# Kernel optimization log

Measured on AMD Instinct MI355X. Metric: run time of the kernel, lower is better.

The kernel has to match this reference:

```python
import jax, jax.numpy as jnp
import numpy as np

V, D, H, L, B, T = 32000, 1024, 16, 4, 2, 2048
DH = D // H
F = 4 * D
EPS = 1e-5


def setup_inputs() -> dict:
    key = jax.random.key(0)
    ks = jax.random.split(key, 16)
    s = 0.02
    n = lambda k, shape: (jax.random.normal(k, shape, jnp.float32) * s)
    inp = {
        "idx": jax.random.randint(ks[0], (B, T), 0, V, dtype=jnp.int64),
        "tok_emb": n(ks[1], (V, D)),
        "pos_emb": n(ks[2], (1, T, D)),
        # per-layer stacked params; Linear weights stored as (in, out)
        "Wq": n(ks[3], (L, D, D)), "bq": jnp.zeros((L, D)),
        "Wk": n(ks[4], (L, D, D)), "bk": jnp.zeros((L, D)),
        "Wv": n(ks[5], (L, D, D)), "bv": jnp.zeros((L, D)),
        "Wo": n(ks[6], (L, D, D)), "bo": jnp.zeros((L, D)),
        "ln1_g": jnp.ones((L, D)), "ln1_b": jnp.zeros((L, D)),
        "W1": n(ks[7], (L, D, F)), "b1": jnp.zeros((L, F)),
        "W2": n(ks[8], (L, F, D)), "b2": jnp.zeros((L, D)),
        "ln2_g": jnp.ones((L, D)), "ln2_b": jnp.zeros((L, D)),
        "lnf_g": jnp.ones((D,)), "lnf_b": jnp.zeros((D,)),
        "lm_W": n(ks[9], (D, V)),
    }
    return inp


def _ln(x, g, b):
    m = jnp.mean(x, axis=-1, keepdims=True)
    v = jnp.mean(jnp.square(x - m), axis=-1, keepdims=True)
    return (x - m) * jax.lax.rsqrt(v + EPS) * g + b


def _band_attn(x, Wq, bq, Wk, bk, Wv, bv, Wo, bo):
    # width-3 causal band: query t attends to keys {t, t-1, t-2}
    b_, t_, _ = x.shape
    q = (x @ Wq + bq).reshape(b_, t_, H, DH)
    k = (x @ Wk + bk).reshape(b_, t_, H, DH)
    v = (x @ Wv + bv).reshape(b_, t_, H, DH)

    def shift(a, o):  # align key at position t-o with query t
        return jnp.pad(a, ((0, 0), (o, 0), (0, 0), (0, 0)))[:, :t_]

    ks_ = jnp.stack([shift(k, o) for o in range(3)], axis=-2)  # (B,T,H,3,DH)
    vs_ = jnp.stack([shift(v, o) for o in range(3)], axis=-2)
    scale = 1.0 / np.sqrt(DH)
    scores = jnp.einsum('bthd,bthod->btho', q, ks_) * scale       # (B,T,H,3)
    pos = jnp.arange(t_)[None, :, None, None]
    off = jnp.arange(3)[None, None, None, :]
    scores = jnp.where(pos >= off, scores, -jnp.inf)
    p = jax.nn.softmax(scores, axis=-1)
    y = jnp.einsum('btho,bthod->bthd', p, vs_).reshape(b_, t_, D)
    return y @ Wo + bo


def reference(idx, tok_emb, pos_emb, Wq, bq, Wk, bk, Wv, bv, Wo, bo,
              ln1_g, ln1_b, W1, b1, W2, b2, ln2_g, ln2_b, lnf_g, lnf_b, lm_W):
    t_ = idx.shape[1]
    x = tok_emb[idx] + pos_emb[:, :t_, :]
    for i in range(L):
        h = _ln(x, ln1_g[i], ln1_b[i])
        x = x + _band_attn(h, Wq[i], bq[i], Wk[i], bk[i], Wv[i], bv[i], Wo[i], bo[i])
        h = _ln(x, ln2_g[i], ln2_b[i])
        h = jax.nn.gelu(h @ W1[i] + b1[i], approximate=False) @ W2[i] + b2[i]
        x = x + h
    x = _ln(x, lnf_g, lnf_b)
    logits = x @ lm_W
    return logits
```

## Files before the change

kernel.cpp:

```cpp
#include <hip/hip_runtime.h>
#include <cstdint>
#include <cstddef>

#define MROWS   4096
#define TSEQ    2048
#define DMODEL  1024
#define NHEAD   16
#define FFN     4096
#define NVOCAB  32000
#define NLAYER  4

typedef float  f32x4  __attribute__((ext_vector_type(4)));
typedef __bf16 bf16x8 __attribute__((ext_vector_type(8)));

__device__ __forceinline__ unsigned short f2bf(float f) {
    unsigned u = __builtin_bit_cast(unsigned, f);
    u += 0x7fffu + ((u >> 16) & 1u);
    return (unsigned short)(u >> 16);
}
__device__ __forceinline__ float bf2f(unsigned short u) {
    return __builtin_bit_cast(float, (unsigned)u << 16);
}

__device__ __forceinline__ float gelu_exact(float v) {
    return 0.5f * v * (1.0f + erff(v * 0.7071067811865476f));
}

__global__ __launch_bounds__(256) void embed_kernel(const int* __restrict__ idx,
                                                    const float* __restrict__ tok,
                                                    const float* __restrict__ pos,
                                                    float* __restrict__ x) {
    int row = blockIdx.x, tid = threadIdx.x;
    int token = idx[row];
    int t = row & (TSEQ - 1);
    float4 a = ((const float4*)(tok + (size_t)token * DMODEL))[tid];
    float4 p = ((const float4*)(pos + (size_t)t * DMODEL))[tid];
    a.x += p.x; a.y += p.y; a.z += p.z; a.w += p.w;
    ((float4*)(x + (size_t)row * DMODEL))[tid] = a;
}

__global__ __launch_bounds__(256) void ln_kernel(const float* __restrict__ x,
                                                 const float* __restrict__ g,
                                                 const float* __restrict__ b,
                                                 unsigned short* __restrict__ out) {
    int row = blockIdx.x, tid = threadIdx.x;
    float4 v = ((const float4*)(x + (size_t)row * DMODEL))[tid];
    float s1 = v.x + v.y + v.z + v.w;
    float s2 = v.x * v.x + v.y * v.y + v.z * v.z + v.w * v.w;
    for (int s = 32; s; s >>= 1) { s1 += __shfl_xor(s1, s); s2 += __shfl_xor(s2, s); }
    __shared__ float red[8];
    int lane = tid & 63, w = tid >> 6;
    if (lane == 0) { red[w] = s1; red[4 + w] = s2; }
    __syncthreads();
    s1 = red[0] + red[1] + red[2] + red[3];
    s2 = red[4] + red[5] + red[6] + red[7];
    float mean = s1 * (1.0f / DMODEL);
    float var  = s2 * (1.0f / DMODEL) - mean * mean;
    float rs   = rsqrtf(var + 1e-5f);
    float4 gv = ((const float4*)g)[tid];
    float4 bv = ((const float4*)b)[tid];
    size_t o = (size_t)row * DMODEL + tid * 4;
    out[o + 0] = f2bf((v.x - mean) * rs * gv.x + bv.x);
    out[o + 1] = f2bf((v.y - mean) * rs * gv.y + bv.y);
    out[o + 2] = f2bf((v.z - mean) * rs * gv.z + bv.z);
    out[o + 3] = f2bf((v.w - mean) * rs * gv.w + bv.w);
}

__global__ __launch_bounds__(256) void transpose_bf16(const float* __restrict__ W,
                                                      unsigned short* __restrict__ WT,
                                                      int K, int ldW) {
    __shared__ float tile[64][65];
    int n0 = blockIdx.x * 64, k0 = blockIdx.y * 64;
    int tid = threadIdx.x;
    int lr4 = tid & 15;
    int rw  = tid >> 4;
#pragma unroll
    for (int p = 0; p < 4; ++p) {
        int k = rw + p * 16;
        float4 v = *(const float4*)(W + (size_t)(k0 + k) * ldW + n0 + lr4 * 4);
        tile[k][lr4 * 4 + 0] = v.x;
        tile[k][lr4 * 4 + 1] = v.y;
        tile[k][lr4 * 4 + 2] = v.z;
        tile[k][lr4 * 4 + 3] = v.w;
    }
    __syncthreads();
    int kc = tid & 15;
    int nr = tid >> 4;
#pragma unroll
    for (int p = 0; p < 4; ++p) {
        int n = nr + p * 16;
        ushort4 o;
        o.x = f2bf(tile[kc * 4 + 0][n]);
        o.y = f2bf(tile[kc * 4 + 1][n]);
        o.z = f2bf(tile[kc * 4 + 2][n]);
        o.w = f2bf(tile[kc * 4 + 3][n]);
        *(ushort4*)(WT + (size_t)(n0 + n) * K + k0 + kc * 4) = o;
    }
}

__global__ __launch_bounds__(256) void pack_qkv_bias(const float* __restrict__ bq,
                                                     const float* __restrict__ bk,
                                                     const float* __restrict__ bv,
                                                     float* __restrict__ dst) {
    int i = blockIdx.x * 256 + threadIdx.x;
    int l = i / 3072, c = i % 3072;
    float v = (c < 1024) ? bq[l * 1024 + c]
            : (c < 2048) ? bk[l * 1024 + c - 1024]
                         : bv[l * 1024 + c - 2048];
    dst[i] = v;
}

__global__ __launch_bounds__(256) void attn_kernel(const unsigned short* __restrict__ qkv,
                                                   unsigned short* __restrict__ y) {
    int wid  = (blockIdx.x * 256 + threadIdx.x) >> 6;
    int lane = threadIdx.x & 63;
    int h = wid & (NHEAD - 1);
    int row = wid >> 4;
    int t = row & (TSEQ - 1);
    const unsigned short* base = qkv + (size_t)row * 3072 + h * 64;
    float qd = bf2f(base[lane]);
    float d0 = qd * bf2f(base[1024 + lane]);
    float d1 = (t >= 1) ? qd * bf2f(base[1024 - 3072 + lane]) : 0.0f;
    float d2 = (t >= 2) ? qd * bf2f(base[1024 - 6144 + lane]) : 0.0f;
    for (int s = 32; s; s >>= 1) {
        d0 += __shfl_xor(d0, s); d1 += __shfl_xor(d1, s); d2 += __shfl_xor(d2, s);
    }
    d0 *= 0.125f; d1 *= 0.125f; d2 *= 0.125f;
    float m = d0;
    if (t >= 1) m = fmaxf(m, d1);
    if (t >= 2) m = fmaxf(m, d2);
    float p0 = expf(d0 - m);
    float p1 = (t >= 1) ? expf(d1 - m) : 0.0f;
    float p2 = (t >= 2) ? expf(d2 - m) : 0.0f;
    float den = p0 + p1 + p2;
    float v0 = bf2f(base[2048 + lane]);
    float v1 = (t >= 1) ? bf2f(base[2048 - 3072 + lane]) : 0.0f;
    float v2 = (t >= 2) ? bf2f(base[2048 - 6144 + lane]) : 0.0f;
    float yv = (p0 * v0 + p1 * v1 + p2 * v2) / den;
    y[(size_t)row * DMODEL + h * 64 + lane] = f2bf(yv);
}

__device__ __forceinline__ void stage_tile(const unsigned short* __restrict__ g,
                                           unsigned short* s, int K, int tid) {
#pragma unroll
    for (int i = 0; i < 4; ++i) {
        int t2 = tid + i * 512;
        int row = t2 >> 3;
        int col = ((t2 & 7) ^ (row & 7)) * 8;
        __builtin_amdgcn_global_load_lds(
            (const __attribute__((address_space(1))) void*)(g + (size_t)row * K + col),
            (__attribute__((address_space(3))) void*)(s + (size_t)t2 * 8), 16, 0, 0);
    }
}

template <int EPI>
__global__ __launch_bounds__(512, 2) void gemm256(const unsigned short* __restrict__ A,
                                                  const unsigned short* __restrict__ BT,
                                                  const float* __restrict__ bias,
                                                  const float* __restrict__ res,
                                                  float* __restrict__ outF,
                                                  unsigned short* __restrict__ outB,
                                                  int M, int N, int K, int ldc) {
    __shared__ unsigned short As[2][256 * 64];
    __shared__ unsigned short Bs[2][256 * 64];
    const int tid = threadIdx.x;
    const int lane = tid & 63, wid = tid >> 6;
    const int wr = wid >> 2, wc = wid & 3;
    const int lr = lane & 15, kq = lane >> 4;

    const int nbn = N >> 8;
    const int nwg = gridDim.x;
    int orig = blockIdx.x;
    int q8 = nwg >> 3, r8 = nwg & 7;
    int xcd = orig & 7, lin = orig >> 3;
    int wg = (xcd < r8 ? xcd * (q8 + 1) : r8 * (q8 + 1) + (xcd - r8) * q8) + lin;
    int bm = wg / nbn, bn = wg % nbn;

    const unsigned short* Ab = A + (size_t)bm * 256 * K;
    const unsigned short* Bb = BT + (size_t)bn * 256 * K;

    const int aBase = (wr * 128 + lr) * 64;
    const int bBase = (wc * 64 + lr) * 64;
    const int c0 = ((0 * 4 + kq) ^ (lr & 7)) * 8;
    const int c1 = ((1 * 4 + kq) ^ (lr & 7)) * 8;

    f32x4 acc[8][4] = {};
    const int nt = K >> 6;

    stage_tile(Ab, &As[0][0], K, tid);
    stage_tile(Bb, &Bs[0][0], K, tid);
    asm volatile("s_waitcnt vmcnt(0)" ::: "memory");
    __syncthreads();

    for (int t = 0; t < nt; ++t) {
        const unsigned short* sA = &As[t & 1][0];
        const unsigned short* sB = &Bs[t & 1][0];
        unsigned short* dA = &As[(t + 1) & 1][0];
        unsigned short* dB = &Bs[(t + 1) & 1][0];
        const bool pf = (t + 1) < nt;
        const unsigned short* gA = Ab + (size_t)(t + 1) * 64;
        const unsigned short* gB = Bb + (size_t)(t + 1) * 64;

        bf16x8 bfr[4][2];
#pragma unroll
        for (int n = 0; n < 4; ++n) {
            bfr[n][0] = *reinterpret_cast<const bf16x8*>(sB + bBase + n * 16 * 64 + c0);
            bfr[n][1] = *reinterpret_cast<const bf16x8*>(sB + bBase + n * 16 * 64 + c1);
        }

#pragma unroll
        for (int q = 0; q < 4; ++q) {
            bf16x8 af[2][2];
#pragma unroll
            for (int jm = 0; jm < 2; ++jm) {
                const int ro = aBase + (q * 32 + jm * 16) * 64;
                af[jm][0] = *reinterpret_cast<const bf16x8*>(sA + ro + c0);
                af[jm][1] = *reinterpret_cast<const bf16x8*>(sA + ro + c1);
            }
            if (q == 0 && pf) stage_tile(gA, dA, K, tid);
            if (q == 1 && pf) stage_tile(gB, dB, K, tid);
            __builtin_amdgcn_s_barrier();
            __builtin_amdgcn_s_setprio(1);
#pragma unroll
            for (int jm = 0; jm < 2; ++jm)
#pragma unroll
                for (int n = 0; n < 4; ++n) {
                    acc[q * 2 + jm][n] = __builtin_amdgcn_mfma_f32_16x16x32_bf16(af[jm][0], bfr[n][0], acc[q * 2 + jm][n], 0, 0, 0);
                    acc[q * 2 + jm][n] = __builtin_amdgcn_mfma_f32_16x16x32_bf16(af[jm][1], bfr[n][1], acc[q * 2 + jm][n], 0, 0, 0);
                }
            __builtin_amdgcn_s_setprio(0);
            if (q < 3) __builtin_amdgcn_s_barrier();
        }
        asm volatile("s_waitcnt vmcnt(0)" ::: "memory");
        __syncthreads();
    }

    const int row0 = bm * 256 + wr * 128;
    const int col0 = bn * 256 + wc * 64;
#pragma unroll
    for (int m = 0; m < 8; ++m) {
#pragma unroll
        for (int n = 0; n < 4; ++n) {
            int col = col0 + n * 16 + lr;
            int rbase = row0 + m * 16 + kq * 4;
            float bb = bias ? bias[col] : 0.0f;
#pragma unroll
            for (int j = 0; j < 4; ++j) {
                size_t off = (size_t)(rbase + j) * ldc + col;
                float v = acc[m][n][j] + bb;
                if (EPI == 1) v += res[off];
                if (EPI == 2)      outB[off] = f2bf(gelu_exact(v));
                else if (EPI == 3) outB[off] = f2bf(v);
                else               outF[off] = v;
            }
        }
    }
}

__device__ __forceinline__ void stage128(const unsigned short* __restrict__ g,
                                         unsigned short* s, int K, int tid) {
#pragma unroll
    for (int i = 0; i < 2; ++i) {
        int t2 = tid + i * 512;
        int row = t2 >> 3;
        int col = ((t2 & 7) ^ (row & 7)) * 8;
        __builtin_amdgcn_global_load_lds(
            (const __attribute__((address_space(1))) void*)(g + (size_t)row * K + col),
            (__attribute__((address_space(3))) void*)(s + (size_t)t2 * 8), 16, 0, 0);
    }
}

template <int EPI>
__global__ __launch_bounds__(512, 2) void gemm128(const unsigned short* __restrict__ A,
                                                  const unsigned short* __restrict__ BT,
                                                  const float* __restrict__ bias,
                                                  const float* __restrict__ res,
                                                  float* __restrict__ outF,
                                                  unsigned short* __restrict__ outB,
                                                  int M, int N, int K, int ldc) {
    __shared__ unsigned short As[3][128 * 64];
    __shared__ unsigned short Bs[3][128 * 64];
    const int tid = threadIdx.x;
    const int lane = tid & 63, wid = tid >> 6;
    const int wr = wid >> 2, wc = wid & 3;
    const int lr = lane & 15, kq = lane >> 4;

    const int nbn = N >> 7;
    const int nwg = gridDim.x;
    int orig = blockIdx.x;
    int q8 = nwg >> 3, r8 = nwg & 7;
    int xcd = orig & 7, lin = orig >> 3;
    int wg = (xcd < r8 ? xcd * (q8 + 1) : r8 * (q8 + 1) + (xcd - r8) * q8) + lin;
    int bm = wg / nbn, bn = wg % nbn;

    const unsigned short* Ab = A + (size_t)bm * 128 * K;
    const unsigned short* Bb = BT + (size_t)bn * 128 * K;

    const int aBase = (wr * 64 + lr) * 64;
    const int bBase = (wc * 32 + lr) * 64;
    const int c0 = (kq ^ (lr & 7)) * 8;
    const int c1 = ((4 + kq) ^ (lr & 7)) * 8;

    f32x4 acc[4][2] = {};
    const int nt = K >> 6;

    stage128(Ab,      &As[0][0], K, tid);
    stage128(Bb,      &Bs[0][0], K, tid);
    stage128(Ab + 64, &As[1][0], K, tid);
    stage128(Bb + 64, &Bs[1][0], K, tid);
    asm volatile("s_waitcnt vmcnt(4)" ::: "memory");
    __builtin_amdgcn_s_barrier();

    for (int t = 0; t < nt; ++t) {
        const unsigned short* sA = &As[t % 3][0];
        const unsigned short* sB = &Bs[t % 3][0];
        const bool pf = (t + 2) < nt;
        unsigned short* dA = &As[(t + 2) % 3][0];
        unsigned short* dB = &Bs[(t + 2) % 3][0];
        const unsigned short* gA = Ab + (size_t)(t + 2) * 64;
        const unsigned short* gB = Bb + (size_t)(t + 2) * 64;

        bf16x8 bfr[2][2];
#pragma unroll
        for (int n = 0; n < 2; ++n) {
            bfr[n][0] = *reinterpret_cast<const bf16x8*>(sB + bBase + n * 16 * 64 + c0);
            bfr[n][1] = *reinterpret_cast<const bf16x8*>(sB + bBase + n * 16 * 64 + c1);
        }
#pragma unroll
        for (int p = 0; p < 2; ++p) {
            bf16x8 af[2][2];
#pragma unroll
            for (int jm = 0; jm < 2; ++jm) {
                const int ro = aBase + ((p * 2 + jm) * 16) * 64;
                af[jm][0] = *reinterpret_cast<const bf16x8*>(sA + ro + c0);
                af[jm][1] = *reinterpret_cast<const bf16x8*>(sA + ro + c1);
            }
            if (pf && p == 0) stage128(gA, dA, K, tid);
            if (pf && p == 1) stage128(gB, dB, K, tid);
            __builtin_amdgcn_s_barrier();
            __builtin_amdgcn_s_setprio(1);
#pragma unroll
            for (int jm = 0; jm < 2; ++jm)
#pragma unroll
                for (int n = 0; n < 2; ++n) {
                    acc[p * 2 + jm][n] = __builtin_amdgcn_mfma_f32_16x16x32_bf16(af[jm][0], bfr[n][0], acc[p * 2 + jm][n], 0, 0, 0);
                    acc[p * 2 + jm][n] = __builtin_amdgcn_mfma_f32_16x16x32_bf16(af[jm][1], bfr[n][1], acc[p * 2 + jm][n], 0, 0, 0);
                }
            __builtin_amdgcn_s_setprio(0);
        }
        if (t + 1 < nt) {
            if (pf) asm volatile("s_waitcnt vmcnt(4)" ::: "memory");
            else    asm volatile("s_waitcnt vmcnt(0)" ::: "memory");
            __builtin_amdgcn_s_barrier();
        }
    }

    const int row0 = bm * 128 + wr * 64;
    const int col0 = bn * 128 + wc * 32;
#pragma unroll
    for (int m = 0; m < 4; ++m) {
#pragma unroll
        for (int n = 0; n < 2; ++n) {
            int col = col0 + n * 16 + lr;
            int rbase = row0 + m * 16 + kq * 4;
            float bb = bias ? bias[col] : 0.0f;
#pragma unroll
            for (int j = 0; j < 4; ++j) {
                size_t off = (size_t)(rbase + j) * ldc + col;
                float v = acc[m][n][j] + bb;
                if (EPI == 1) v += res[off];
                if (EPI == 2)      outB[off] = f2bf(gelu_exact(v));
                else if (EPI == 3) outB[off] = f2bf(v);
                else               outF[off] = v;
            }
        }
    }
}

extern "C" void kernel_launch(void* const* d_in, const int* in_sizes, int n_in,
                              void* d_out, int out_size, void* d_ws, size_t ws_size,
                              hipStream_t stream) {
    const int*   idx  = (const int*)d_in[0];
    const float* tok  = (const float*)d_in[1];
    const float* pos  = (const float*)d_in[2];
    const float* Wq   = (const float*)d_in[3];
    const float* bq   = (const float*)d_in[4];
    const float* Wk   = (const float*)d_in[5];
    const float* bk   = (const float*)d_in[6];
    const float* Wv   = (const float*)d_in[7];
    const float* bv   = (const float*)d_in[8];
    const float* Wo   = (const float*)d_in[9];
    const float* bo   = (const float*)d_in[10];
    const float* ln1g = (const float*)d_in[11];
    const float* ln1b = (const float*)d_in[12];
    const float* W1   = (const float*)d_in[13];
    const float* b1   = (const float*)d_in[14];
    const float* W2   = (const float*)d_in[15];
    const float* b2   = (const float*)d_in[16];
    const float* ln2g = (const float*)d_in[17];
    const float* ln2b = (const float*)d_in[18];
    const float* lnfg = (const float*)d_in[19];
    const float* lnfb = (const float*)d_in[20];
    const float* lmW  = (const float*)d_in[21];

    char* ws = (char*)d_ws;
    unsigned short* wbuf  = (unsigned short*)(ws);
    unsigned short* hbuf  = (unsigned short*)(ws + (16u << 20));
    unsigned short* ybuf  = (unsigned short*)(ws + (24u << 20));
    unsigned short* xfbuf = (unsigned short*)(ws + (32u << 20));
    float*          bqkv  = (float*)(ws + (40u << 20));

    float* outF = (float*)d_out;
    float* xbuf = outF;
    unsigned short* qkv = (unsigned short*)((char*)d_out + (16ull << 20));
    unsigned short* hidden = (unsigned short*)((char*)d_out + (64ull << 20));

    embed_kernel<<<MROWS, 256, 0, stream>>>(idx, tok, pos, xbuf);
    pack_qkv_bias<<<(NLAYER * 3072) / 256, 256, 0, stream>>>(bq, bk, bv, bqkv);

    for (int l = 0; l < NLAYER; l++) {
        const size_t wl = (size_t)l * DMODEL * DMODEL;
        ln_kernel<<<MROWS, 256, 0, stream>>>(xbuf, ln1g + l * DMODEL, ln1b + l * DMODEL, hbuf);

        transpose_bf16<<<dim3(16, 16), 256, 0, stream>>>(Wq + wl, wbuf,                           DMODEL, DMODEL);
        transpose_bf16<<<dim3(16, 16), 256, 0, stream>>>(Wk + wl, wbuf + (size_t)DMODEL * DMODEL, DMODEL, DMODEL);
        transpose_bf16<<<dim3(16, 16), 256, 0, stream>>>(Wv + wl, wbuf + 2ull * DMODEL * DMODEL,  DMODEL, DMODEL);
        gemm256<3><<<dim3((3072 / 256) * (MROWS / 256)), 512, 0, stream>>>(
            hbuf, wbuf, bqkv + l * 3072, nullptr, nullptr, qkv, MROWS, 3072, DMODEL, 3072);

        attn_kernel<<<MROWS * NHEAD / 4, 256, 0, stream>>>(qkv, ybuf);

        transpose_bf16<<<dim3(16, 16), 256, 0, stream>>>(Wo + wl, wbuf, DMODEL, DMODEL);
        gemm128<1><<<dim3((DMODEL / 128) * (MROWS / 128)), 512, 0, stream>>>(
            ybuf, wbuf, bo + l * DMODEL, xbuf, xbuf, nullptr, MROWS, DMODEL, DMODEL, DMODEL);

        ln_kernel<<<MROWS, 256, 0, stream>>>(xbuf, ln2g + l * DMODEL, ln2b + l * DMODEL, hbuf);

        transpose_bf16<<<dim3(FFN / 64, DMODEL / 64), 256, 0, stream>>>(W1 + (size_t)l * DMODEL * FFN, wbuf, DMODEL, FFN);
        gemm256<2><<<dim3((FFN / 256) * (MROWS / 256)), 512, 0, stream>>>(
            hbuf, wbuf, b1 + l * FFN, nullptr, nullptr, hidden, MROWS, FFN, DMODEL, FFN);

        transpose_bf16<<<dim3(DMODEL / 64, FFN / 64), 256, 0, stream>>>(W2 + (size_t)l * FFN * DMODEL, wbuf, FFN, DMODEL);
        gemm128<1><<<dim3((DMODEL / 128) * (MROWS / 128)), 512, 0, stream>>>(
            hidden, wbuf, b2 + l * DMODEL, xbuf, xbuf, nullptr, MROWS, DMODEL, FFN, DMODEL);
    }

    ln_kernel<<<MROWS, 256, 0, stream>>>(xbuf, lnfg, lnfb, xfbuf);

    const int NCHUNK = 6400;
    for (int c = 0; c < NVOCAB / NCHUNK; c++) {
        int n0 = c * NCHUNK;
        transpose_bf16<<<dim3(NCHUNK / 64, DMODEL / 64), 256, 0, stream>>>(lmW + n0, wbuf, DMODEL, NVOCAB);
        gemm256<0><<<dim3((NCHUNK / 256) * (MROWS / 256)), 512, 0, stream>>>(
            xfbuf, wbuf, nullptr, nullptr, outF + n0, nullptr, MROWS, NCHUNK, DMODEL, NVOCAB);
    }
}
```

Before: 1.447 ms.

## Split GEMM K-tile into halves with finer-grained async staging, fuse QKV transpose, unchunk LM head

The 256x256 GEMM now stages each 64-wide K tile as two 32-wide halves with a new swizzle. It uses partial vmcnt waits so loads for the next tile overlap the MFMA work on the current half, replacing the full waitcnt and syncthreads per tile. The three QKV weight transposes are merged into one 3D-grid launch. When the workspace is large enough, the LM head transposes and multiplies the whole vocabulary in one launch instead of five chunks. The partial-wait pipelining depends on exact load counts and could race if those counts are wrong.

```diff
diff --git a/kernel.cpp b/kernel.cpp
--- a/kernel.cpp
+++ b/kernel.cpp
@@ -98,6 +98,39 @@
     }
 }
 
+__global__ __launch_bounds__(256) void transpose_qkv(const float* __restrict__ Wq,
+                                                     const float* __restrict__ Wk,
+                                                     const float* __restrict__ Wv,
+                                                     unsigned short* __restrict__ WT) {
+    __shared__ float tile[64][65];
+    const float* W = (blockIdx.z == 0) ? Wq : (blockIdx.z == 1) ? Wk : Wv;
+    unsigned short* dst = WT + (size_t)blockIdx.z * DMODEL * DMODEL;
+    int n0 = blockIdx.x * 64, k0 = blockIdx.y * 64;
+    int tid = threadIdx.x;
+    int lr4 = tid & 15, rw = tid >> 4;
+#pragma unroll
+    for (int p = 0; p < 4; ++p) {
+        int k = rw + p * 16;
+        float4 v = *(const float4*)(W + (size_t)(k0 + k) * DMODEL + n0 + lr4 * 4);
+        tile[k][lr4 * 4 + 0] = v.x;
+        tile[k][lr4 * 4 + 1] = v.y;
+        tile[k][lr4 * 4 + 2] = v.z;
+        tile[k][lr4 * 4 + 3] = v.w;
+    }
+    __syncthreads();
+    int kc = tid & 15, nr = tid >> 4;
+#pragma unroll
+    for (int p = 0; p < 4; ++p) {
+        int n = nr + p * 16;
+        ushort4 o;
+        o.x = f2bf(tile[kc * 4 + 0][n]);
+        o.y = f2bf(tile[kc * 4 + 1][n]);
+        o.z = f2bf(tile[kc * 4 + 2][n]);
+        o.w = f2bf(tile[kc * 4 + 3][n]);
+        *(ushort4*)(dst + (size_t)(n0 + n) * DMODEL + k0 + kc * 4) = o;
+    }
+}
+
 __global__ __launch_bounds__(256) void pack_qkv_bias(const float* __restrict__ bq,
                                                      const float* __restrict__ bk,
                                                      const float* __restrict__ bv,
@@ -140,16 +173,17 @@
     y[(size_t)row * DMODEL + h * 64 + lane] = f2bf(yv);
 }
 
-__device__ __forceinline__ void stage_tile(const unsigned short* __restrict__ g,
-                                           unsigned short* s, int K, int tid) {
-#pragma unroll
-    for (int i = 0; i < 4; ++i) {
-        int t2 = tid + i * 512;
-        int row = t2 >> 3;
-        int col = ((t2 & 7) ^ (row & 7)) * 8;
+__device__ __forceinline__ void stage_kh(const unsigned short* __restrict__ g,
+                                         unsigned short* region, int K, int kh, int tid) {
+#pragma unroll
+    for (int i = 0; i < 2; ++i) {
+        int pc = i * 512 + tid;
+        int line = pc >> 3, slot = pc & 7;
+        int r  = line * 2 + (slot >> 2);
+        int cl = (slot & 3) ^ (line & 3);
         __builtin_amdgcn_global_load_lds(
-            (const __attribute__((address_space(1))) void*)(g + (size_t)row * K + col),
-            (__attribute__((address_space(3))) void*)(s + (size_t)t2 * 8), 16, 0, 0);
+            (const __attribute__((address_space(1))) void*)(g + (size_t)r * K + kh * 32 + cl * 8),
+            (__attribute__((address_space(3))) void*)(region + (size_t)pc * 8), 16, 0, 0);
     }
 }
 
@@ -161,8 +195,8 @@
                                                   float* __restrict__ outF,
                                                   unsigned short* __restrict__ outB,
                                                   int M, int N, int K, int ldc) {
-    __shared__ unsigned short As[2][256 * 64];
-    __shared__ unsigned short Bs[2][256 * 64];
+    __shared__ unsigned short As[2][2][8192];
+    __shared__ unsigned short Bs[2][2][8192];
     const int tid = threadIdx.x;
     const int lane = tid & 63, wid = tid >> 6;
     const int wr = wid >> 2, wc = wid & 3;
@@ -179,60 +213,61 @@
     const unsigned short* Ab = A + (size_t)bm * 256 * K;
     const unsigned short* Bb = BT + (size_t)bn * 256 * K;
 
-    const int aBase = (wr * 128 + lr) * 64;
-    const int bBase = (wc * 64 + lr) * 64;
-    const int c0 = ((0 * 4 + kq) ^ (lr & 7)) * 8;
-    const int c1 = ((1 * 4 + kq) ^ (lr & 7)) * 8;
+    const int slot = ((lane & 1) << 2) | (kq ^ ((lr >> 1) & 3));
+    const int laneOff = ((lr >> 1) << 6) + slot * 8;
 
     f32x4 acc[8][4] = {};
     const int nt = K >> 6;
 
-    stage_tile(Ab, &As[0][0], K, tid);
-    stage_tile(Bb, &Bs[0][0], K, tid);
-    asm volatile("s_waitcnt vmcnt(0)" ::: "memory");
-    __syncthreads();
+    stage_kh(Ab, &As[0][0][0], K, 0, tid);
+    stage_kh(Bb, &Bs[0][0][0], K, 0, tid);
+    stage_kh(Ab, &As[0][1][0], K, 1, tid);
+    stage_kh(Bb, &Bs[0][1][0], K, 1, tid);
 
     for (int t = 0; t < nt; ++t) {
-        const unsigned short* sA = &As[t & 1][0];
-        const unsigned short* sB = &Bs[t & 1][0];
-        unsigned short* dA = &As[(t + 1) & 1][0];
-        unsigned short* dB = &Bs[(t + 1) & 1][0];
+        const int buf = t & 1;
         const bool pf = (t + 1) < nt;
         const unsigned short* gA = Ab + (size_t)(t + 1) * 64;
         const unsigned short* gB = Bb + (size_t)(t + 1) * 64;
 
-        bf16x8 bfr[4][2];
-#pragma unroll
-        for (int n = 0; n < 4; ++n) {
-            bfr[n][0] = *reinterpret_cast<const bf16x8*>(sB + bBase + n * 16 * 64 + c0);
-            bfr[n][1] = *reinterpret_cast<const bf16x8*>(sB + bBase + n * 16 * 64 + c1);
-        }
-
-#pragma unroll
-        for (int q = 0; q < 4; ++q) {
-            bf16x8 af[2][2];
-#pragma unroll
-            for (int jm = 0; jm < 2; ++jm) {
-                const int ro = aBase + (q * 32 + jm * 16) * 64;
-                af[jm][0] = *reinterpret_cast<const bf16x8*>(sA + ro + c0);
-                af[jm][1] = *reinterpret_cast<const bf16x8*>(sA + ro + c1);
-            }
-            if (q == 0 && pf) stage_tile(gA, dA, K, tid);
-            if (q == 1 && pf) stage_tile(gB, dB, K, tid);
+#pragma unroll
+        for (int kh = 0; kh < 2; ++kh) {
+            if (kh == 0 || pf) asm volatile("s_waitcnt vmcnt(4)" ::: "memory");
+            else               asm volatile("s_waitcnt vmcnt(0)" ::: "memory");
             __builtin_amdgcn_s_barrier();
+            if (pf) stage_kh(gA, &As[buf ^ 1][kh][0], K, kh, tid);
+
+            const unsigned short* rA = &As[buf][kh][0];
+            const unsigned short* rB = &Bs[buf][kh][0];
+            bf16x8 bfrag[4];
+#pragma unroll
+            for (int n = 0; n < 4; ++n)
+                bfrag[n] = *(const bf16x8*)(rB + wc * 2048 + n * 512 + laneOff);
+            bf16x8 afrag[4];
+#pragma unroll
+            for (int j = 0; j < 4; ++j)
+                afrag[j] = *(const bf16x8*)(rA + wr * 4096 + j * 512 + laneOff);
             __builtin_amdgcn_s_setprio(1);
 #pragma unroll
-            for (int jm = 0; jm < 2; ++jm)
-#pragma unroll
-                for (int n = 0; n < 4; ++n) {
-                    acc[q * 2 + jm][n] = __builtin_amdgcn_mfma_f32_16x16x32_bf16(af[jm][0], bfr[n][0], acc[q * 2 + jm][n], 0, 0, 0);
-                    acc[q * 2 + jm][n] = __builtin_amdgcn_mfma_f32_16x16x32_bf16(af[jm][1], bfr[n][1], acc[q * 2 + jm][n], 0, 0, 0);
-                }
+            for (int j = 0; j < 4; ++j)
+#pragma unroll
+                for (int n = 0; n < 4; ++n)
+                    acc[j][n] = __builtin_amdgcn_mfma_f32_16x16x32_bf16(afrag[j], bfrag[n], acc[j][n], 0, 0, 0);
             __builtin_amdgcn_s_setprio(0);
-            if (q < 3) __builtin_amdgcn_s_barrier();
-        }
-        asm volatile("s_waitcnt vmcnt(0)" ::: "memory");
-        __syncthreads();
+
+            __builtin_amdgcn_s_barrier();
+            if (pf) stage_kh(gB, &Bs[buf ^ 1][kh][0], K, kh, tid);
+#pragma unroll
+            for (int j = 0; j < 4; ++j)
+                afrag[j] = *(const bf16x8*)(rA + wr * 4096 + (4 + j) * 512 + laneOff);
+            __builtin_amdgcn_s_setprio(1);
+#pragma unroll
+            for (int j = 0; j < 4; ++j)
+#pragma unroll
+                for (int n = 0; n < 4; ++n)
+                    acc[4 + j][n] = __builtin_amdgcn_mfma_f32_16x16x32_bf16(afrag[j], bfrag[n], acc[4 + j][n], 0, 0, 0);
+            __builtin_amdgcn_s_setprio(0);
+        }
     }
 
     const int row0 = bm * 256 + wr * 128;
@@ -403,12 +438,27 @@
     const float* lnfb = (const float*)d_in[20];
     const float* lmW  = (const float*)d_in[21];
 
+    const bool bigws = ws_size >= (92ull << 20);
+
     char* ws = (char*)d_ws;
-    unsigned short* wbuf  = (unsigned short*)(ws);
-    unsigned short* hbuf  = (unsigned short*)(ws + (16u << 20));
-    unsigned short* ybuf  = (unsigned short*)(ws + (24u << 20));
-    unsigned short* xfbuf = (unsigned short*)(ws + (32u << 20));
-    float*          bqkv  = (float*)(ws + (40u << 20));
+    unsigned short* wbuf;
+    unsigned short* hbuf;
+    unsigned short* ybuf;
+    unsigned short* xfbuf;
+    float*          bqkv;
+    if (bigws) {
+        wbuf  = (unsigned short*)(ws);
+        hbuf  = (unsigned short*)(ws + (63ull << 20));
+        ybuf  = (unsigned short*)(ws + (71ull << 20));
+        xfbuf = (unsigned short*)(ws + (79ull << 20));
+        bqkv  = (float*)(ws + (87ull << 20));
+    } else {
+        wbuf  = (unsigned short*)(ws);
+        hbuf  = (unsigned short*)(ws + (16u << 20));
+        ybuf  = (unsigned short*)(ws + (24u << 20));
+        xfbuf = (unsigned short*)(ws + (32u << 20));
+        bqkv  = (float*)(ws + (40u << 20));
+    }
 
     float* outF = (float*)d_out;
     float* xbuf = outF;
@@ -422,9 +472,7 @@
         const size_t wl = (size_t)l * DMODEL * DMODEL;
         ln_kernel<<<MROWS, 256, 0, stream>>>(xbuf, ln1g + l * DMODEL, ln1b + l * DMODEL, hbuf);
 
-        transpose_bf16<<<dim3(16, 16), 256, 0, stream>>>(Wq + wl, wbuf,                           DMODEL, DMODEL);
-        transpose_bf16<<<dim3(16, 16), 256, 0, stream>>>(Wk + wl, wbuf + (size_t)DMODEL * DMODEL, DMODEL, DMODEL);
-        transpose_bf16<<<dim3(16, 16), 256, 0, stream>>>(Wv + wl, wbuf + 2ull * DMODEL * DMODEL,  DMODEL, DMODEL);
+        transpose_qkv<<<dim3(16, 16, 3), 256, 0, stream>>>(Wq + wl, Wk + wl, Wv + wl, wbuf);
         gemm256<3><<<dim3((3072 / 256) * (MROWS / 256)), 512, 0, stream>>>(
             hbuf, wbuf, bqkv + l * 3072, nullptr, nullptr, qkv, MROWS, 3072, DMODEL, 3072);
 
@@ -447,11 +495,17 @@
 
     ln_kernel<<<MROWS, 256, 0, stream>>>(xbuf, lnfg, lnfb, xfbuf);
 
-    const int NCHUNK = 6400;
-    for (int c = 0; c < NVOCAB / NCHUNK; c++) {
-        int n0 = c * NCHUNK;
-        transpose_bf16<<<dim3(NCHUNK / 64, DMODEL / 64), 256, 0, stream>>>(lmW + n0, wbuf, DMODEL, NVOCAB);
-        gemm256<0><<<dim3((NCHUNK / 256) * (MROWS / 256)), 512, 0, stream>>>(
-            xfbuf, wbuf, nullptr, nullptr, outF + n0, nullptr, MROWS, NCHUNK, DMODEL, NVOCAB);
-    }
-}
+    if (bigws) {
+        transpose_bf16<<<dim3(NVOCAB / 64, DMODEL / 64), 256, 0, stream>>>(lmW, wbuf, DMODEL, NVOCAB);
+        gemm256<0><<<dim3((NVOCAB / 256) * (MROWS / 256)), 512, 0, stream>>>(
+            xfbuf, wbuf, nullptr, nullptr, outF, nullptr, MROWS, NVOCAB, DMODEL, NVOCAB);
+    } else {
+        const int NCHUNK = 6400;
+        for (int c = 0; c < NVOCAB / NCHUNK; c++) {
+            int n0 = c * NCHUNK;
+            transpose_bf16<<<dim3(NCHUNK / 64, DMODEL / 64), 256, 0, stream>>>(lmW + n0, wbuf, DMODEL, NVOCAB);
+            gemm256<0><<<dim3((NCHUNK / 256) * (MROWS / 256)), 512, 0, stream>>>(
+                xfbuf, wbuf, nullptr, nullptr, outF + n0, nullptr, MROWS, NCHUNK, DMODEL, NVOCAB);
+        }
+    }
+}
```

Result: slower. 1.487 ms (+2.8%).
